# Kernel tuning notes

Hardware: AMD Instinct MI355X
Metric: run time of the kernel (lower is better)

The kernel has to match this reference:

```python
import jax, jax.numpy as jnp
import numpy as np

H = 512
B = 64
S = 2048

def setup_inputs() -> dict:
    key = jax.random.key(0)
    ks = jax.random.split(key, 7)
    s = 1.0 / np.sqrt(H)
    return {
        "query": jax.random.normal(ks[0], (B, H), dtype=jnp.float32),
        "ref": jax.random.normal(ks[1], (B, S, H), dtype=jnp.float32),
        "Wq": jax.random.uniform(ks[2], (H, H), dtype=jnp.float32, minval=-s, maxval=s),
        "bq": jax.random.uniform(ks[3], (H,), dtype=jnp.float32, minval=-s, maxval=s),
        "Wr": jax.random.uniform(ks[4], (H, H), dtype=jnp.float32, minval=-s, maxval=s),
        "br": jax.random.uniform(ks[5], (H,), dtype=jnp.float32, minval=-s, maxval=s),
        "V": jax.random.uniform(ks[6], (H,), dtype=jnp.float32, minval=-s, maxval=s),
    }

def reference(query, ref, Wq, bq, Wr, br, V):
    # W_ref is Conv1d(H, H, kernel=1) applied to ref permuted to [B,H,S];
    # a 1x1 conv is a per-position GEMM: out[b,o,s] = sum_h Wr[o,h] * ref[b,s,h] + br[o]
    ref_t = jnp.einsum('bsh,oh->bos', ref, Wr) + br[None, :, None]  # [B,H,S]
    q = query @ Wq.T + bq                                            # [B,H]
    # logits[b,s] = V . tanh(q[b,:] + ref_t[b,:,s])
    logits = jnp.einsum('h,bhs->bs', V, jnp.tanh(q[:, :, None] + ref_t))  # [B,S]
    # use_tanh=False -> no C*tanh clipping
    return ref_t, logits
```

## Files before the change

kernel.cpp:

```cpp
#include <hip/hip_runtime.h>

constexpr int Hd = 512;
constexpr int Bd = 64;
constexpr int Sd = 2048;

constexpr int BM = 128;
constexpr int BN = 128;
constexpr int BK = 32;
constexpr int LDP = BK + 4;

typedef __bf16 bf16x8 __attribute__((ext_vector_type(8)));
typedef float  f32x4  __attribute__((ext_vector_type(4)));
typedef unsigned short u16x8 __attribute__((ext_vector_type(8)));

__device__ __forceinline__ unsigned short f2bf(float f){
  __bf16 h = (__bf16)f;
  return __builtin_bit_cast(unsigned short, h);
}

__device__ __forceinline__ float fast_tanh(float x){
  float e = __expf(2.0f * x);
  return 1.0f - 2.0f * __builtin_amdgcn_rcpf(e + 1.0f);
}

__global__ __launch_bounds__(256) void prologue_kernel(const float* __restrict__ Wr,
                                                       unsigned short* __restrict__ Wrb,
                                                       const float* __restrict__ query,
                                                       const float* __restrict__ Wq,
                                                       const float* __restrict__ bq,
                                                       float* __restrict__ qout){
  if (blockIdx.x < 128){
    int base = (blockIdx.x*256 + (int)threadIdx.x) * 8;
    f32x4 v0 = *(const f32x4*)(Wr + base);
    f32x4 v1 = *(const f32x4*)(Wr + base + 4);
    u16x8 o;
    o[0]=f2bf(v0[0]); o[1]=f2bf(v0[1]); o[2]=f2bf(v0[2]); o[3]=f2bf(v0[3]);
    o[4]=f2bf(v1[0]); o[5]=f2bf(v1[1]); o[6]=f2bf(v1[2]); o[7]=f2bf(v1[3]);
    *(u16x8*)(Wrb + base) = o;
  } else {
    int b   = blockIdx.x - 128;
    int tid = threadIdx.x;
    __shared__ float qs[Hd];
    for (int i = tid; i < Hd; i += 256) qs[i] = query[b*Hd + i];
    __syncthreads();
    for (int o = tid; o < Hd; o += 256){
      const float* w = Wq + (size_t)o*Hd;
      float s = 0.f;
      #pragma unroll 4
      for (int k = 0; k < Hd; k += 4){
        f32x4 wv = *(const f32x4*)(w + k);
        s += wv[0]*qs[k] + wv[1]*qs[k+1] + wv[2]*qs[k+2] + wv[3]*qs[k+3];
      }
      qout[b*Hd + o] = s + bq[o];
    }
  }
}

__global__ __launch_bounds__(256, 3) void fused_kernel(const float* __restrict__ ref,
                                                       const unsigned short* __restrict__ Wrb,
                                                       const float* __restrict__ br,
                                                       const float* __restrict__ V,
                                                       const float* __restrict__ qbuf,
                                                       float* __restrict__ out,
                                                       float* __restrict__ logits){
  const int bid = blockIdx.x;
  const int wid = (bid & 7) * (gridDim.x >> 3) + (bid >> 3);
  const int mt  = wid & 3;
  const int nt  = (wid >> 2) & 15;
  const int bb  = wid >> 6;
  const int m0  = mt * BM;
  const int n0  = nt * BN;

  const int tid  = threadIdx.x;
  const int lane = tid & 63;
  const int wave = tid >> 6;
  const int wm   = wave >> 1;
  const int wn   = wave & 1;

  __shared__ unsigned short As[2][BM][LDP];
  __shared__ unsigned short Bs[2][BN][LDP];

  f32x4 acc[4][4];
  #pragma unroll
  for (int i = 0; i < 4; ++i)
    #pragma unroll
    for (int j = 0; j < 4; ++j)
      acc[i][j] = f32x4{0.f, 0.f, 0.f, 0.f};

  const int ar = tid >> 1;
  const int ak = (tid & 1) * 16;
  const int sr = tid >> 3;
  const int sk = (tid & 7) * 4;

  const unsigned short* Ag = Wrb + (size_t)(m0 + ar)*Hd + ak;
  const float*          Bg = ref + ((size_t)bb*Sd + (n0 + sr))*Hd + sk;

  const int rofs = lane & 15;
  const int koff = (lane >> 4) * 8;

  u16x8 Ar0, Ar1;
  f32x4 Br0[4], Br1[4];

  Ar0 = *(const u16x8*)(Ag);
  Ar1 = *(const u16x8*)(Ag + 8);
  #pragma unroll
  for (int it = 0; it < 4; ++it) Br0[it] = *(const f32x4*)(Bg + (size_t)it*32*Hd);
  *(u16x8*)(&As[0][ar][ak])     = Ar0;
  *(u16x8*)(&As[0][ar][ak + 8]) = Ar1;
  Ar0 = *(const u16x8*)(Ag + BK);
  Ar1 = *(const u16x8*)(Ag + BK + 8);
  #pragma unroll
  for (int it = 0; it < 4; ++it) Br1[it] = *(const f32x4*)(Bg + (size_t)it*32*Hd + BK);
  #pragma unroll
  for (int it = 0; it < 4; ++it){
    uint2 pk;
    pk.x = (unsigned)f2bf(Br0[it][0]) | ((unsigned)f2bf(Br0[it][1]) << 16);
    pk.y = (unsigned)f2bf(Br0[it][2]) | ((unsigned)f2bf(Br0[it][3]) << 16);
    *(uint2*)(&Bs[0][sr + it*32][sk]) = pk;
  }
  #pragma unroll
  for (int it = 0; it < 4; ++it) Br0[it] = *(const f32x4*)(Bg + (size_t)it*32*Hd + 2*BK);
  asm volatile("s_waitcnt lgkmcnt(0)" ::: "memory");
  __builtin_amdgcn_s_barrier();

  auto step = [&](int cur, int t, f32x4 (&Br)[4]){
    const int nxt = cur ^ 1;
    bf16x8 a[4], b[4];
    #pragma unroll
    for (int mi = 0; mi < 4; ++mi)
      a[mi] = *(const bf16x8*)(&As[cur][wm*64 + mi*16 + rofs][koff]);
    #pragma unroll
    for (int ni = 0; ni < 4; ++ni)
      b[ni] = *(const bf16x8*)(&Bs[cur][wn*64 + ni*16 + rofs][koff]);

    *(u16x8*)(&As[nxt][ar][ak])     = Ar0;
    *(u16x8*)(&As[nxt][ar][ak + 8]) = Ar1;
    #pragma unroll
    for (int it = 0; it < 4; ++it){
      uint2 pk;
      pk.x = (unsigned)f2bf(Br[it][0]) | ((unsigned)f2bf(Br[it][1]) << 16);
      pk.y = (unsigned)f2bf(Br[it][2]) | ((unsigned)f2bf(Br[it][3]) << 16);
      *(uint2*)(&Bs[nxt][sr + it*32][sk]) = pk;
    }

    int ka = t + 2; ka = (ka > 15 ? 15 : ka) * BK;
    int kb = t + 3; kb = (kb > 15 ? 15 : kb) * BK;
    Ar0 = *(const u16x8*)(Ag + ka);
    Ar1 = *(const u16x8*)(Ag + ka + 8);
    #pragma unroll
    for (int it = 0; it < 4; ++it) Br[it] = *(const f32x4*)(Bg + (size_t)it*32*Hd + kb);

    asm volatile("s_waitcnt lgkmcnt(0)" ::: "memory");
    #pragma unroll
    for (int mi = 0; mi < 4; ++mi)
      #pragma unroll
      for (int ni = 0; ni < 4; ++ni)
        acc[mi][ni] = __builtin_amdgcn_mfma_f32_16x16x32_bf16(a[mi], b[ni], acc[mi][ni], 0, 0, 0);
    __builtin_amdgcn_s_barrier();
  };

  #pragma unroll 1
  for (int t2 = 0; t2 < 8; ++t2){
    step(0, t2*2,     Br1);
    step(1, t2*2 + 1, Br0);
  }

  const int col0 = n0 + wn*64;
  const int row0 = m0 + wm*64;
  const int cl   = lane & 15;
  const int rgrp = (lane >> 4) * 4;
  const float* qrow = qbuf + bb*Hd;
  float colsum[4] = {0.f, 0.f, 0.f, 0.f};
  float* outb = out + (size_t)bb*Hd*Sd;

  #pragma unroll
  for (int mi = 0; mi < 4; ++mi){
    #pragma unroll
    for (int j = 0; j < 4; ++j){
      int o = row0 + mi*16 + rgrp + j;
      float brv = br[o];
      float qv  = qrow[o];
      float vv  = V[o];
      float* orow = outb + (size_t)o*Sd + col0;
      #pragma unroll
      for (int ni = 0; ni < 4; ++ni){
        float c = acc[mi][ni][j] + brv;
        __builtin_nontemporal_store(c, &orow[ni*16 + cl]);
        colsum[ni] += vv * fast_tanh(qv + c);
      }
    }
  }

  #pragma unroll
  for (int ni = 0; ni < 4; ++ni){
    colsum[ni] += __shfl_xor(colsum[ni], 16);
    colsum[ni] += __shfl_xor(colsum[ni], 32);
  }
  if (lane < 16){
    float* lrow = logits + (size_t)bb*Sd + col0;
    #pragma unroll
    for (int ni = 0; ni < 4; ++ni)
      atomicAdd(lrow + ni*16 + cl, colsum[ni]);
  }
}

extern "C" void kernel_launch(void* const* d_in, const int* in_sizes, int n_in,
                              void* d_out, int out_size, void* d_ws, size_t ws_size,
                              hipStream_t stream){
  const float* query = (const float*)d_in[0];
  const float* ref   = (const float*)d_in[1];
  const float* Wq    = (const float*)d_in[2];
  const float* bq    = (const float*)d_in[3];
  const float* Wr    = (const float*)d_in[4];
  const float* br    = (const float*)d_in[5];
  const float* V     = (const float*)d_in[6];

  float* out    = (float*)d_out;
  float* logits = out + (size_t)Bd*Hd*Sd;
  float* qbuf   = (float*)d_ws;
  unsigned short* Wrb = (unsigned short*)((char*)d_ws + 128*1024);

  hipMemsetAsync(logits, 0, (size_t)Bd*Sd*sizeof(float), stream);
  prologue_kernel<<<192, 256, 0, stream>>>(Wr, Wrb, query, Wq, bq, qbuf);

  fused_kernel<<<Bd*64, 256, 0, stream>>>(ref, Wrb, br, V, qbuf, out, logits);
}
```

Before: 217.2 us.

## Halve N tile, single-buffer swizzled LDS, raise occupancy to four blocks

Shrinks the N tile from 128 to 64 and doubles the grid. LDS drops from double-buffered padded arrays to one XOR-swizzled buffer, with two barriers per K step and a register-staged prefetch one step ahead. Launch bounds rise to four blocks per CU, aiming for more latency hiding and fewer bank conflicts. In exchange the fp32 ref traffic relative to MFMA work doubles, because each block now reads ref for 128 rows but covers half the columns, and the extra barrier adds synchronisation cost.

```diff
diff --git a/kernel.cpp b/kernel.cpp
--- a/kernel.cpp
+++ b/kernel.cpp
@@ -5,9 +5,8 @@
 constexpr int Sd = 2048;
 
 constexpr int BM = 128;
-constexpr int BN = 128;
+constexpr int BN = 64;
 constexpr int BK = 32;
-constexpr int LDP = BK + 4;
 
 typedef __bf16 bf16x8 __attribute__((ext_vector_type(8)));
 typedef float  f32x4  __attribute__((ext_vector_type(4)));
@@ -21,6 +20,10 @@
 __device__ __forceinline__ float fast_tanh(float x){
   float e = __expf(2.0f * x);
   return 1.0f - 2.0f * __builtin_amdgcn_rcpf(e + 1.0f);
+}
+
+__device__ __forceinline__ int swz(int row, int slot){
+  return row*32 + ((slot ^ (row & 3)) << 3);
 }
 
 __global__ __launch_bounds__(256) void prologue_kernel(const float* __restrict__ Wr,
@@ -56,7 +59,9 @@
   }
 }
 
-__global__ __launch_bounds__(256, 3) void fused_kernel(const float* __restrict__ ref,
+struct SReg { u16x8 a0, a1; f32x4 b0, b1; };
+
+__global__ __launch_bounds__(256, 4) void fused_kernel(const float* __restrict__ ref,
                                                        const unsigned short* __restrict__ Wrb,
                                                        const float* __restrict__ br,
                                                        const float* __restrict__ V,
@@ -66,8 +71,8 @@
   const int bid = blockIdx.x;
   const int wid = (bid & 7) * (gridDim.x >> 3) + (bid >> 3);
   const int mt  = wid & 3;
-  const int nt  = (wid >> 2) & 15;
-  const int bb  = wid >> 6;
+  const int nt  = (wid >> 2) & 31;
+  const int bb  = wid >> 7;
   const int m0  = mt * BM;
   const int n0  = nt * BN;
 
@@ -77,100 +82,83 @@
   const int wm   = wave >> 1;
   const int wn   = wave & 1;
 
-  __shared__ unsigned short As[2][BM][LDP];
-  __shared__ unsigned short Bs[2][BN][LDP];
-
-  f32x4 acc[4][4];
+  __shared__ unsigned short As[BM*32];
+  __shared__ unsigned short Bs[BN*32];
+
+  f32x4 acc[4][2];
   #pragma unroll
   for (int i = 0; i < 4; ++i)
     #pragma unroll
-    for (int j = 0; j < 4; ++j)
+    for (int j = 0; j < 2; ++j)
       acc[i][j] = f32x4{0.f, 0.f, 0.f, 0.f};
 
   const int ar = tid >> 1;
-  const int ak = (tid & 1) * 16;
-  const int sr = tid >> 3;
-  const int sk = (tid & 7) * 4;
-
-  const unsigned short* Ag = Wrb + (size_t)(m0 + ar)*Hd + ak;
+  const int as0 = (tid & 1) * 2;
+  const int sr = tid >> 2;
+  const int sk = (tid & 3) * 8;
+
+  const unsigned short* Ag = Wrb + (size_t)(m0 + ar)*Hd + as0*8;
   const float*          Bg = ref + ((size_t)bb*Sd + (n0 + sr))*Hd + sk;
 
+  const int aw0 = swz(ar, as0), aw1 = swz(ar, as0 + 1);
+  const int bw  = swz(sr, tid & 3);
+
   const int rofs = lane & 15;
-  const int koff = (lane >> 4) * 8;
-
-  u16x8 Ar0, Ar1;
-  f32x4 Br0[4], Br1[4];
-
-  Ar0 = *(const u16x8*)(Ag);
-  Ar1 = *(const u16x8*)(Ag + 8);
-  #pragma unroll
-  for (int it = 0; it < 4; ++it) Br0[it] = *(const f32x4*)(Bg + (size_t)it*32*Hd);
-  *(u16x8*)(&As[0][ar][ak])     = Ar0;
-  *(u16x8*)(&As[0][ar][ak + 8]) = Ar1;
-  Ar0 = *(const u16x8*)(Ag + BK);
-  Ar1 = *(const u16x8*)(Ag + BK + 8);
-  #pragma unroll
-  for (int it = 0; it < 4; ++it) Br1[it] = *(const f32x4*)(Bg + (size_t)it*32*Hd + BK);
-  #pragma unroll
-  for (int it = 0; it < 4; ++it){
-    uint2 pk;
-    pk.x = (unsigned)f2bf(Br0[it][0]) | ((unsigned)f2bf(Br0[it][1]) << 16);
-    pk.y = (unsigned)f2bf(Br0[it][2]) | ((unsigned)f2bf(Br0[it][3]) << 16);
-    *(uint2*)(&Bs[0][sr + it*32][sk]) = pk;
-  }
-  #pragma unroll
-  for (int it = 0; it < 4; ++it) Br0[it] = *(const f32x4*)(Bg + (size_t)it*32*Hd + 2*BK);
-  asm volatile("s_waitcnt lgkmcnt(0)" ::: "memory");
-  __builtin_amdgcn_s_barrier();
-
-  auto step = [&](int cur, int t, f32x4 (&Br)[4]){
-    const int nxt = cur ^ 1;
-    bf16x8 a[4], b[4];
+  const int slot = lane >> 4;
+
+  SReg S0, S1;
+
+  auto issue = [&](SReg& S, int kt){
+    S.a0 = *(const u16x8*)(Ag + kt);
+    S.a1 = *(const u16x8*)(Ag + kt + 8);
+    S.b0 = *(const f32x4*)(Bg + kt);
+    S.b1 = *(const f32x4*)(Bg + kt + 4);
+  };
+  auto write_stage = [&](const SReg& S){
+    *(u16x8*)(&As[aw0]) = S.a0;
+    *(u16x8*)(&As[aw1]) = S.a1;
+    uint4 pk;
+    pk.x = (unsigned)f2bf(S.b0[0]) | ((unsigned)f2bf(S.b0[1]) << 16);
+    pk.y = (unsigned)f2bf(S.b0[2]) | ((unsigned)f2bf(S.b0[3]) << 16);
+    pk.z = (unsigned)f2bf(S.b1[0]) | ((unsigned)f2bf(S.b1[1]) << 16);
+    pk.w = (unsigned)f2bf(S.b1[2]) | ((unsigned)f2bf(S.b1[3]) << 16);
+    *(uint4*)(&Bs[bw]) = pk;
+  };
+  auto halfstep = [&](const SReg& Sw, SReg& Sn, int t){
+    write_stage(Sw);
+    int kn = t + 1; kn = (kn > 15 ? 15 : kn) * BK;
+    issue(Sn, kn);
+    asm volatile("s_waitcnt lgkmcnt(0)" ::: "memory");
+    __builtin_amdgcn_s_barrier();
+    bf16x8 a[4], b[2];
     #pragma unroll
     for (int mi = 0; mi < 4; ++mi)
-      a[mi] = *(const bf16x8*)(&As[cur][wm*64 + mi*16 + rofs][koff]);
-    #pragma unroll
-    for (int ni = 0; ni < 4; ++ni)
-      b[ni] = *(const bf16x8*)(&Bs[cur][wn*64 + ni*16 + rofs][koff]);
-
-    *(u16x8*)(&As[nxt][ar][ak])     = Ar0;
-    *(u16x8*)(&As[nxt][ar][ak + 8]) = Ar1;
-    #pragma unroll
-    for (int it = 0; it < 4; ++it){
-      uint2 pk;
-      pk.x = (unsigned)f2bf(Br[it][0]) | ((unsigned)f2bf(Br[it][1]) << 16);
-      pk.y = (unsigned)f2bf(Br[it][2]) | ((unsigned)f2bf(Br[it][3]) << 16);
-      *(uint2*)(&Bs[nxt][sr + it*32][sk]) = pk;
-    }
-
-    int ka = t + 2; ka = (ka > 15 ? 15 : ka) * BK;
-    int kb = t + 3; kb = (kb > 15 ? 15 : kb) * BK;
-    Ar0 = *(const u16x8*)(Ag + ka);
-    Ar1 = *(const u16x8*)(Ag + ka + 8);
-    #pragma unroll
-    for (int it = 0; it < 4; ++it) Br[it] = *(const f32x4*)(Bg + (size_t)it*32*Hd + kb);
-
-    asm volatile("s_waitcnt lgkmcnt(0)" ::: "memory");
+      a[mi] = *(const bf16x8*)(&As[swz(wm*64 + mi*16 + rofs, slot)]);
+    #pragma unroll
+    for (int ni = 0; ni < 2; ++ni)
+      b[ni] = *(const bf16x8*)(&Bs[swz(wn*32 + ni*16 + rofs, slot)]);
     #pragma unroll
     for (int mi = 0; mi < 4; ++mi)
       #pragma unroll
-      for (int ni = 0; ni < 4; ++ni)
+      for (int ni = 0; ni < 2; ++ni)
         acc[mi][ni] = __builtin_amdgcn_mfma_f32_16x16x32_bf16(a[mi], b[ni], acc[mi][ni], 0, 0, 0);
+    asm volatile("s_waitcnt lgkmcnt(0)" ::: "memory");
     __builtin_amdgcn_s_barrier();
   };
 
+  issue(S0, 0);
   #pragma unroll 1
   for (int t2 = 0; t2 < 8; ++t2){
-    step(0, t2*2,     Br1);
-    step(1, t2*2 + 1, Br0);
-  }
-
-  const int col0 = n0 + wn*64;
+    halfstep(S0, S1, t2*2);
+    halfstep(S1, S0, t2*2 + 1);
+  }
+
+  const int col0 = n0 + wn*32;
   const int row0 = m0 + wm*64;
   const int cl   = lane & 15;
   const int rgrp = (lane >> 4) * 4;
   const float* qrow = qbuf + bb*Hd;
-  float colsum[4] = {0.f, 0.f, 0.f, 0.f};
+  float colsum[2] = {0.f, 0.f};
   float* outb = out + (size_t)bb*Hd*Sd;
 
   #pragma unroll
@@ -183,7 +171,7 @@
       float vv  = V[o];
       float* orow = outb + (size_t)o*Sd + col0;
       #pragma unroll
-      for (int ni = 0; ni < 4; ++ni){
+      for (int ni = 0; ni < 2; ++ni){
         float c = acc[mi][ni][j] + brv;
         __builtin_nontemporal_store(c, &orow[ni*16 + cl]);
         colsum[ni] += vv * fast_tanh(qv + c);
@@ -192,14 +180,14 @@
   }
 
   #pragma unroll
-  for (int ni = 0; ni < 4; ++ni){
+  for (int ni = 0; ni < 2; ++ni){
     colsum[ni] += __shfl_xor(colsum[ni], 16);
     colsum[ni] += __shfl_xor(colsum[ni], 32);
   }
   if (lane < 16){
     float* lrow = logits + (size_t)bb*Sd + col0;
     #pragma unroll
-    for (int ni = 0; ni < 4; ++ni)
+    for (int ni = 0; ni < 2; ++ni)
       atomicAdd(lrow + ni*16 + cl, colsum[ni]);
   }
 }
@@ -223,5 +211,5 @@
   hipMemsetAsync(logits, 0, (size_t)Bd*Sd*sizeof(float), stream);
   prologue_kernel<<<192, 256, 0, stream>>>(Wr, Wrb, query, Wq, bq, qbuf);
 
-  fused_kernel<<<Bd*64, 256, 0, stream>>>(ref, Wrb, br, V, qbuf, out, logits);
-}
+  fused_kernel<<<Bd*4*32, 256, 0, stream>>>(ref, Wrb, br, V, qbuf, out, logits);
+}
```

After: 231.8 us. +6.7%, slower.

## Switch to single LDS buffer with two-deep register prefetch pipeline

Applied to the files above, without the earlier changes.

The double-buffered shared memory tiles are replaced by a single LDS stage. Global loads are now kept two iterations ahead in two register sets. Each step writes a staged register set to LDS, issues the next global load, synchronizes, reads fragments and runs the MFMAs, then synchronizes again. This halves LDS use, likely to raise occupancy, but adds a second barrier per k-step and serializes the LDS write with compute.

```diff
diff --git a/kernel.cpp b/kernel.cpp
--- a/kernel.cpp
+++ b/kernel.cpp
@@ -56,6 +56,8 @@
   }
 }
 
+struct SReg { u16x8 a0, a1; f32x4 b[4]; };
+
 __global__ __launch_bounds__(256, 3) void fused_kernel(const float* __restrict__ ref,
                                                        const unsigned short* __restrict__ Wrb,
                                                        const float* __restrict__ br,
@@ -77,8 +79,8 @@
   const int wm   = wave >> 1;
   const int wn   = wave & 1;
 
-  __shared__ unsigned short As[2][BM][LDP];
-  __shared__ unsigned short Bs[2][BN][LDP];
+  __shared__ unsigned short As[BM][LDP];
+  __shared__ unsigned short Bs[BN][LDP];
 
   f32x4 acc[4][4];
   #pragma unroll
@@ -98,71 +100,53 @@
   const int rofs = lane & 15;
   const int koff = (lane >> 4) * 8;
 
-  u16x8 Ar0, Ar1;
-  f32x4 Br0[4], Br1[4];
-
-  Ar0 = *(const u16x8*)(Ag);
-  Ar1 = *(const u16x8*)(Ag + 8);
-  #pragma unroll
-  for (int it = 0; it < 4; ++it) Br0[it] = *(const f32x4*)(Bg + (size_t)it*32*Hd);
-  *(u16x8*)(&As[0][ar][ak])     = Ar0;
-  *(u16x8*)(&As[0][ar][ak + 8]) = Ar1;
-  Ar0 = *(const u16x8*)(Ag + BK);
-  Ar1 = *(const u16x8*)(Ag + BK + 8);
-  #pragma unroll
-  for (int it = 0; it < 4; ++it) Br1[it] = *(const f32x4*)(Bg + (size_t)it*32*Hd + BK);
-  #pragma unroll
-  for (int it = 0; it < 4; ++it){
-    uint2 pk;
-    pk.x = (unsigned)f2bf(Br0[it][0]) | ((unsigned)f2bf(Br0[it][1]) << 16);
-    pk.y = (unsigned)f2bf(Br0[it][2]) | ((unsigned)f2bf(Br0[it][3]) << 16);
-    *(uint2*)(&Bs[0][sr + it*32][sk]) = pk;
-  }
-  #pragma unroll
-  for (int it = 0; it < 4; ++it) Br0[it] = *(const f32x4*)(Bg + (size_t)it*32*Hd + 2*BK);
-  asm volatile("s_waitcnt lgkmcnt(0)" ::: "memory");
-  __builtin_amdgcn_s_barrier();
-
-  auto step = [&](int cur, int t, f32x4 (&Br)[4]){
-    const int nxt = cur ^ 1;
-    bf16x8 a[4], b[4];
-    #pragma unroll
-    for (int mi = 0; mi < 4; ++mi)
-      a[mi] = *(const bf16x8*)(&As[cur][wm*64 + mi*16 + rofs][koff]);
-    #pragma unroll
-    for (int ni = 0; ni < 4; ++ni)
-      b[ni] = *(const bf16x8*)(&Bs[cur][wn*64 + ni*16 + rofs][koff]);
-
-    *(u16x8*)(&As[nxt][ar][ak])     = Ar0;
-    *(u16x8*)(&As[nxt][ar][ak + 8]) = Ar1;
+  SReg S0, S1;
+
+  auto issue = [&](SReg& S, int kt){
+    S.a0 = *(const u16x8*)(Ag + kt);
+    S.a1 = *(const u16x8*)(Ag + kt + 8);
+    #pragma unroll
+    for (int it = 0; it < 4; ++it) S.b[it] = *(const f32x4*)(Bg + (size_t)it*32*Hd + kt);
+  };
+  auto write_stage = [&](const SReg& S){
+    *(u16x8*)(&As[ar][ak])     = S.a0;
+    *(u16x8*)(&As[ar][ak + 8]) = S.a1;
     #pragma unroll
     for (int it = 0; it < 4; ++it){
       uint2 pk;
-      pk.x = (unsigned)f2bf(Br[it][0]) | ((unsigned)f2bf(Br[it][1]) << 16);
-      pk.y = (unsigned)f2bf(Br[it][2]) | ((unsigned)f2bf(Br[it][3]) << 16);
-      *(uint2*)(&Bs[nxt][sr + it*32][sk]) = pk;
+      pk.x = (unsigned)f2bf(S.b[it][0]) | ((unsigned)f2bf(S.b[it][1]) << 16);
+      pk.y = (unsigned)f2bf(S.b[it][2]) | ((unsigned)f2bf(S.b[it][3]) << 16);
+      *(uint2*)(&Bs[sr + it*32][sk]) = pk;
     }
-
-    int ka = t + 2; ka = (ka > 15 ? 15 : ka) * BK;
-    int kb = t + 3; kb = (kb > 15 ? 15 : kb) * BK;
-    Ar0 = *(const u16x8*)(Ag + ka);
-    Ar1 = *(const u16x8*)(Ag + ka + 8);
-    #pragma unroll
-    for (int it = 0; it < 4; ++it) Br[it] = *(const f32x4*)(Bg + (size_t)it*32*Hd + kb);
-
+  };
+  auto step = [&](SReg& S, int t){
+    write_stage(S);
+    int kn = t + 2; kn = (kn > 15 ? 15 : kn) * BK;
+    issue(S, kn);
     asm volatile("s_waitcnt lgkmcnt(0)" ::: "memory");
+    __builtin_amdgcn_s_barrier();
+    bf16x8 a[4], b[4];
+    #pragma unroll
+    for (int mi = 0; mi < 4; ++mi)
+      a[mi] = *(const bf16x8*)(&As[wm*64 + mi*16 + rofs][koff]);
+    #pragma unroll
+    for (int ni = 0; ni < 4; ++ni)
+      b[ni] = *(const bf16x8*)(&Bs[wn*64 + ni*16 + rofs][koff]);
     #pragma unroll
     for (int mi = 0; mi < 4; ++mi)
       #pragma unroll
       for (int ni = 0; ni < 4; ++ni)
         acc[mi][ni] = __builtin_amdgcn_mfma_f32_16x16x32_bf16(a[mi], b[ni], acc[mi][ni], 0, 0, 0);
+    asm volatile("s_waitcnt lgkmcnt(0)" ::: "memory");
     __builtin_amdgcn_s_barrier();
   };
 
+  issue(S0, 0);
+  issue(S1, BK);
   #pragma unroll 1
   for (int t2 = 0; t2 < 8; ++t2){
-    step(0, t2*2,     Br1);
-    step(1, t2*2 + 1, Br0);
+    step(S0, t2*2);
+    step(S1, t2*2 + 1);
   }
 
   const int col0 = n0 + wn*64;
```

Measured after the change: 203.9 us. -6.1%, faster.
